# Optimization experiments

Measured on AMD Instinct MI355X. Metric: run time of the kernel, lower is better.

The kernel has to match this reference:

```python
import jax, jax.numpy as jnp
import numpy as np

N_NODES = 50000
N_EDGES = 1600000
E_DIM = 128
N_LAYERS = 3
N_GRAPHS = 32


def setup_inputs() -> dict:
    key = jax.random.key(0)
    ks = jax.random.split(key, 12)
    x = jax.random.normal(ks[0], (N_NODES,), dtype=jnp.float32)
    edge_index = jax.random.randint(ks[1], (2, N_EDGES), 0, N_NODES, dtype=jnp.int32)
    batch = jnp.sort(jax.random.randint(ks[2], (N_NODES,), 0, N_GRAPHS, dtype=jnp.int32))
    s_in = 1.0  # fan_in = 1 for the first linear
    s_e = 1.0 / np.sqrt(E_DIM)
    lin_w = jax.random.normal(ks[3], (1, E_DIM), jnp.float32) * s_in
    lin_b = jax.random.normal(ks[4], (E_DIM,), jnp.float32) * 0.01
    gcn_w = jax.random.normal(ks[5], (N_LAYERS, E_DIM, E_DIM), jnp.float32) * s_e
    gcn_b = jax.random.normal(ks[6], (N_LAYERS, E_DIM), jnp.float32) * 0.01
    r1_w = jax.random.normal(ks[7], (E_DIM, E_DIM), jnp.float32) * s_e
    r1_b = jax.random.normal(ks[8], (E_DIM,), jnp.float32) * 0.01
    r2_w = jax.random.normal(ks[9], (E_DIM, 1), jnp.float32) * s_e
    r2_b = jax.random.normal(ks[10], (1,), jnp.float32) * 0.01
    return {"x": x, "edge_index": edge_index, "batch": batch,
            "lin_w": lin_w, "lin_b": lin_b, "gcn_w": gcn_w, "gcn_b": gcn_b,
            "r1_w": r1_w, "r1_b": r1_b, "r2_w": r2_w, "r2_b": r2_b}


def reference(x, edge_index, batch, lin_w, lin_b, gcn_w, gcn_b, r1_w, r1_b, r2_w, r2_b):
    # input embedding: x.view(-1, 1) @ W + b -> [N, E]
    h = x.reshape(-1, 1) @ lin_w + lin_b

    # GCN normalization (add self-loops, symmetric deg^-1/2 norm) — structure is
    # identical across layers, so compute once.
    loops = jnp.arange(N_NODES, dtype=edge_index.dtype)
    src = jnp.concatenate([edge_index[0], loops])
    dst = jnp.concatenate([edge_index[1], loops])
    deg = jax.ops.segment_sum(jnp.ones(src.shape[0], h.dtype), dst, num_segments=N_NODES)
    dinv = jnp.where(deg > 0, jax.lax.rsqrt(deg), 0.0)
    norm = (dinv[src] * dinv[dst])[:, None]  # [E+N, 1]

    # NOTE: original calls x.relu() without assignment -> no activation (faithful).
    for l in range(N_LAYERS):
        h = h @ gcn_w[l]                                        # [N, E]
        h = jax.ops.segment_sum(h[src] * norm, dst, num_segments=N_NODES) + gcn_b[l]

    # global_add_pool over graphs
    pooled = jax.ops.segment_sum(h, batch, num_segments=N_GRAPHS)  # [G, E]
    hr = jnp.tanh(pooled @ r1_w + r1_b)
    return hr @ r2_w + r2_b  # [G, 1]
```

## Files before the change

kernel.cpp:

```cpp
#include <hip/hip_runtime.h>
#include <math.h>

#define NGRAPH 32
#define CAP 10240
#define EPT 8
#define EPB (256 * EPT)
#define BLK 256

__device__ __forceinline__ int block_scan_excl(int v, int tid, int* wsum, int& total) {
    int x = v;
#pragma unroll
    for (int d = 1; d < 64; d <<= 1) {
        int t = __shfl_up(x, d);
        if ((tid & 63) >= d) x += t;
    }
    if ((tid & 63) == 63) wsum[tid >> 6] = x;
    __syncthreads();
    if (tid == 0) {
        int a = 0;
#pragma unroll
        for (int i = 0; i < 4; i++) { int t = wsum[i]; wsum[i] = a; a += t; }
        wsum[4] = a;
    }
    __syncthreads();
    total = wsum[4];
    return x - v + wsum[tid >> 6];
}

__global__ __launch_bounds__(256) void k_part_chain(
        const int* __restrict__ src, const int* __restrict__ dst,
        int* __restrict__ gcursor, unsigned int* __restrict__ packed, int E, int nchunk,
        const float* __restrict__ lin_w, const float* __restrict__ lin_b,
        const float* __restrict__ gcn_w, const float* __restrict__ gcn_b,
        float* __restrict__ chainv) {
    __shared__ union {
        struct { unsigned int ldsbuf[EPB]; int hist[256], lofs[256], lcur[256], base[256], wsum[5]; } p;
        struct { float v4[512]; } c;
    } sm;
    int tid = threadIdx.x;

    if ((int)blockIdx.x == nchunk) {
        float* v4 = sm.c.v4;
        int j = tid & 127, gg = tid >> 7;
        if (tid < 128) {
            v4[tid]       = lin_w[tid];
            v4[128 + tid] = lin_b[tid];
            v4[256 + tid] = gcn_b[tid];
            v4[384 + tid] = gcn_b[128 + tid];
        }
        __syncthreads();
        for (int l = 0; l < 3; l++) {
            const float* W = gcn_w + l * 128 * 128;
            float a0 = 0.f, a1 = 0.f;
            for (int k0 = 0; k0 < 128; k0 += 16) {
                float wreg[16];
#pragma unroll
                for (int t = 0; t < 16; t++) wreg[t] = W[(k0 + t) * 128 + j];
#pragma unroll
                for (int t = 0; t < 16; t++) {
                    a0 += v4[gg * 128 + k0 + t] * wreg[t];
                    a1 += v4[(gg + 2) * 128 + k0 + t] * wreg[t];
                }
            }
            __syncthreads();
            v4[gg * 128 + j] = a0;
            bool upd = (gg == 0) ? (l >= 1) : (l >= 2);
            if (upd) v4[(gg + 2) * 128 + j] = a1;
            __syncthreads();
        }
        chainv[tid]       = v4[tid];
        chainv[256 + tid] = v4[256 + tid];
        return;
    }

    int e0 = blockIdx.x * EPB;
    sm.p.hist[tid] = 0;
    __syncthreads();
    int d_[EPT], s_[EPT];
#pragma unroll
    for (int c = 0; c < EPT / 4; c++) {
        int e = e0 + c * 1024 + (tid << 2);
        if (e + 3 < E) {
            int4 dv = *(const int4*)&dst[e];
            int4 sv = *(const int4*)&src[e];
            d_[4*c+0] = dv.x; d_[4*c+1] = dv.y; d_[4*c+2] = dv.z; d_[4*c+3] = dv.w;
            s_[4*c+0] = sv.x; s_[4*c+1] = sv.y; s_[4*c+2] = sv.z; s_[4*c+3] = sv.w;
            atomicAdd(&sm.p.hist[dv.x >> 8], 1);
            atomicAdd(&sm.p.hist[dv.y >> 8], 1);
            atomicAdd(&sm.p.hist[dv.z >> 8], 1);
            atomicAdd(&sm.p.hist[dv.w >> 8], 1);
        } else {
#pragma unroll
            for (int k = 0; k < 4; k++) {
                int ee = e + k;
                if (ee < E) {
                    d_[4*c+k] = dst[ee]; s_[4*c+k] = src[ee];
                    atomicAdd(&sm.p.hist[d_[4*c+k] >> 8], 1);
                } else {
                    d_[4*c+k] = -1;
                }
            }
        }
    }
    __syncthreads();
    int v = sm.p.hist[tid];
    int total;
    int excl = block_scan_excl(v, tid, sm.p.wsum, total);
    sm.p.lofs[tid] = excl;
    sm.p.lcur[tid] = excl;
    if (v > 0) sm.p.base[tid] = tid * CAP + atomicAdd(&gcursor[tid], v);
    __syncthreads();
#pragma unroll
    for (int c = 0; c < EPT; c++) {
        int dd = d_[c];
        if (dd >= 0) {
            int bk = dd >> 8;
            int slot = atomicAdd(&sm.p.lcur[bk], 1);
            sm.p.ldsbuf[slot] = ((unsigned int)bk << 24) | ((unsigned int)s_[c] << 8)
                              | (unsigned int)(dd & 255);
        }
    }
    __syncthreads();
    for (int i = tid; i < total; i += BLK) {
        unsigned int w = sm.p.ldsbuf[i];
        int bk = w >> 24;
        packed[sm.p.base[bk] + (i - sm.p.lofs[bk])] = w & 0xFFFFFFu;
    }
}

__global__ __launch_bounds__(256) void k_bucket(
        const unsigned int* __restrict__ packed, const int* __restrict__ gcursor,
        const float* __restrict__ x, const int* __restrict__ batch,
        int* __restrict__ offs, int* __restrict__ deg,
        float* __restrict__ dinv, float2* __restrict__ q0,
        float2* __restrict__ q1, float2* __restrict__ q2,
        unsigned short* __restrict__ csr, float* __restrict__ S, int N) {
    __shared__ unsigned int buf[CAP];
    __shared__ __align__(16) unsigned short lcsr[CAP];
    __shared__ int cnt[256], lcur[256], wsum[5];
    __shared__ float cs[NGRAPH];
    int tid = threadIdx.x;
    int b = blockIdx.x;
    int start = b * CAP;
    int len = gcursor[b];
    cnt[tid] = 0;
    if (tid < NGRAPH) cs[tid] = 0.f;
    __syncthreads();
    for (int e = tid; e < len; e += BLK) {
        unsigned int w = packed[start + e];
        buf[e] = w;
        atomicAdd(&cnt[w & 255], 1);
    }
    __syncthreads();
    int v = cnt[tid];
    int vp = (v + 7) & ~7;
    int total;
    int excl = block_scan_excl(vp, tid, wsum, total);
    lcur[tid] = excl;
    int node = b * 256 + tid;
    if (node < N) {
        deg[node] = v;
        offs[node] = start + excl;
        float dv = rsqrtf((float)(v + 1));
        dinv[node] = dv;
        q0[node] = make_float2(x[node] * dv, dv);
        atomicAdd(&cs[batch[node]], 1.f);
        for (int p = v; p < vp; p++)
            lcsr[excl + p] = (unsigned short)N;
    }
    if (b == 0 && tid == 0) {
        q0[N] = make_float2(0.f, 0.f);
        q1[N] = make_float2(0.f, 0.f);
        q2[N] = make_float2(0.f, 0.f);
    }
    __syncthreads();
    for (int e = tid; e < len; e += BLK) {
        unsigned int w = buf[e];
        lcsr[atomicAdd(&lcur[w & 255], 1)] = (unsigned short)(w >> 8);
    }
    if (tid < NGRAPH && cs[tid] != 0.f) atomicAdd(&S[tid], cs[tid]);
    __syncthreads();
    const uint4* ls = (const uint4*)lcsr;
    uint4* gs = (uint4*)&csr[start];
    for (int i = tid; i < (total >> 3); i += BLK) gs[i] = ls[i];
}

template <int WRITE_Q>
__global__ __launch_bounds__(256) void k_hop(
        const float2* __restrict__ qin, float2* __restrict__ outv,
        const unsigned short* __restrict__ csr,
        const int* __restrict__ offs, const int* __restrict__ deg,
        const float* __restrict__ dinv, int N) {
    int tid  = threadIdx.x;
    int lane = tid & 3;
    int node = blockIdx.x * 64 + (tid >> 2);
    if (node >= N) return;
    int e = offs[node], ne = deg[node];
    float sx = 0.0f, su = 0.0f;
    for (int j = 8 * lane; j < ne; j += 32) {
        ushort4 c0 = *(const ushort4*)&csr[e + j];
        ushort4 c1 = *(const ushort4*)&csr[e + j + 4];
        float2 a0 = qin[c0.x], a1 = qin[c0.y], a2 = qin[c0.z], a3 = qin[c0.w];
        float2 b0 = qin[c1.x], b1 = qin[c1.y], b2 = qin[c1.z], b3 = qin[c1.w];
        sx += ((a0.x + a1.x) + (a2.x + a3.x)) + ((b0.x + b1.x) + (b2.x + b3.x));
        su += ((a0.y + a1.y) + (a2.y + a3.y)) + ((b0.y + b1.y) + (b2.y + b3.y));
    }
#pragma unroll
    for (int m = 2; m > 0; m >>= 1) {
        sx += __shfl_xor(sx, m);
        su += __shfl_xor(su, m);
    }
    if (lane == 0) {
        float2 qs = qin[node];
        float dv = dinv[node];
        float px = dv * (sx + qs.x), pu = dv * (su + qs.y);
        if (WRITE_Q) outv[node] = make_float2(px * dv, pu * dv);
        else         outv[node] = make_float2(px, pu);
    }
}

__global__ __launch_bounds__(256) void k_mlp(
        const float* __restrict__ S, const float* __restrict__ chainv,
        const float2* __restrict__ q1, const float2* __restrict__ q2,
        const float2* __restrict__ p3, const float* __restrict__ dinv,
        const float* __restrict__ gcn_b,
        const float* __restrict__ r1_w, const float* __restrict__ r1_b,
        const float* __restrict__ r2_w, const float* __restrict__ r2_b,
        float* __restrict__ out, int N) {
    __shared__ float rw[128 * 128];
    __shared__ float pl[128], red[128];
    __shared__ float cnts[NGRAPH];
    __shared__ float r4[4 * 128];
    int tid = threadIdx.x;
    int g = blockIdx.x;
    {
        const float4* Rg = (const float4*)r1_w;
        float4* Rs = (float4*)rw;
#pragma unroll
        for (int i = 0; i < 16; i++) Rs[tid + i * 256] = Rg[tid + i * 256];
    }
    if (tid < NGRAPH) cnts[tid] = S[tid];
    __syncthreads();
    int r0 = 0;
    for (int i = 0; i < g; i++) r0 += (int)cnts[i];
    int cnt = (int)cnts[g];
    int r1e = r0 + cnt;
    float su1 = 0.f, su2 = 0.f, su3 = 0.f, sv3 = 0.f;
    for (int n = r0 + tid; n < r1e; n += BLK) {
        float inv = 1.0f / dinv[n];
        su1 += q1[n].y * inv;
        su2 += q2[n].y * inv;
        float2 p = p3[n];
        su3 += p.y; sv3 += p.x;
    }
#pragma unroll
    for (int m = 32; m > 0; m >>= 1) {
        su1 += __shfl_xor(su1, m);
        su2 += __shfl_xor(su2, m);
        su3 += __shfl_xor(su3, m);
        sv3 += __shfl_xor(sv3, m);
    }
    int wv = tid >> 6;
    if ((tid & 63) == 0) {
        r4[wv] = su1; r4[4 + wv] = su2; r4[8 + wv] = su3; r4[12 + wv] = sv3;
    }
    __syncthreads();
    su1 = r4[0] + r4[1] + r4[2] + r4[3];
    su2 = r4[4] + r4[5] + r4[6] + r4[7];
    su3 = r4[8] + r4[9] + r4[10] + r4[11];
    sv3 = r4[12] + r4[13] + r4[14] + r4[15];
    const float* b3 = gcn_b + 2 * 128;
    if (tid < 128)
        pl[tid] = sv3 * chainv[tid] + su3 * chainv[128 + tid] + su2 * chainv[256 + tid]
                + su1 * chainv[384 + tid] + (float)cnt * b3[tid];
    __syncthreads();
    int j = tid & 127, half = tid >> 7;
    float acc = 0.f;
#pragma unroll 8
    for (int kk = 0; kk < 64; kk++) {
        int k = half * 64 + kk;
        acc += pl[k] * rw[k * 128 + j];
    }
    r4[half * 128 + j] = acc;
    __syncthreads();
    if (tid < 128) {
        float a = r4[tid] + r4[128 + tid] + r1_b[tid];
        red[tid] = tanhf(a) * r2_w[tid];
    }
    __syncthreads();
    for (int sft = 64; sft > 0; sft >>= 1) {
        if (tid < sft) red[tid] += red[tid + sft];
        __syncthreads();
    }
    if (tid == 0) out[g] = red[0] + r2_b[0];
}

extern "C" void kernel_launch(void* const* d_in, const int* in_sizes, int n_in,
                              void* d_out, int out_size, void* d_ws, size_t ws_size,
                              hipStream_t stream) {
    const float* x     = (const float*)d_in[0];
    const int*   eidx  = (const int*)d_in[1];
    const int*   batch = (const int*)d_in[2];
    const float* lin_w = (const float*)d_in[3];
    const float* lin_b = (const float*)d_in[4];
    const float* gcn_w = (const float*)d_in[5];
    const float* gcn_b = (const float*)d_in[6];
    const float* r1_w  = (const float*)d_in[7];
    const float* r1_b  = (const float*)d_in[8];
    const float* r2_w  = (const float*)d_in[9];
    const float* r2_b  = (const float*)d_in[10];

    const int N = in_sizes[0];
    const int E = in_sizes[1] / 2;
    const int* src = eidx;
    const int* dst = eidx + E;
    const int NB = (N + 255) / 256;

    char* w = (char*)d_ws;
    float2* q0      = (float2*)w; w += (size_t)(N + 2) * 8;
    float2* q1      = (float2*)w; w += (size_t)(N + 2) * 8;
    float2* q2      = (float2*)w; w += (size_t)(N + 2) * 8;
    float2* p3      = (float2*)w; w += (size_t)(N + 2) * 8;
    unsigned int* packed = (unsigned int*)w; w += (size_t)256 * CAP * 4;
    int*    offs    = (int*)w;    w += (size_t)N * 4;
    int*    deg     = (int*)w;    w += (size_t)N * 4;
    float*  dinv    = (float*)w;  w += (size_t)N * 4;
    int*    gcursor = (int*)w;    w += 256 * 4;
    float*  S       = (float*)w;  w += 64 * 4;
    float*  chainv  = (float*)w;  w += 512 * 4;
    unsigned short* csr = (unsigned short*)w; w += (size_t)256 * CAP * 2 + 256;

    hipMemsetAsync(gcursor, 0, 256 * 4 + 64 * 4, stream);

    const int nchunk = (E + EPB - 1) / EPB;
    k_part_chain<<<nchunk + 1, 256, 0, stream>>>(src, dst, gcursor, packed, E, nchunk,
                                                 lin_w, lin_b, gcn_w, gcn_b, chainv);
    k_bucket<<<NB, 256, 0, stream>>>(packed, gcursor, x, batch, offs, deg, dinv,
                                     q0, q1, q2, csr, S, N);

    const int hop_blocks = (N + 63) / 64;
    k_hop<1><<<hop_blocks, 256, 0, stream>>>(q0, q1, csr, offs, deg, dinv, N);
    k_hop<1><<<hop_blocks, 256, 0, stream>>>(q1, q2, csr, offs, deg, dinv, N);
    k_hop<0><<<hop_blocks, 256, 0, stream>>>(q2, p3, csr, offs, deg, dinv, N);

    k_mlp<<<NGRAPH, 256, 0, stream>>>(S, chainv, q1, q2, p3, dinv, gcn_b,
                                      r1_w, r1_b, r2_w, r2_b, (float*)d_out, N);
}
```

Measured before the change: 155.7 us.

## Fuse per-graph pooling reductions into hop kernels via shared-memory atomics

The per-graph sums of q1, q2 and the final hop output are now accumulated inside the second and third hop kernels. Each block reduces into shared-memory bins keyed by the node's batch id, then adds the bins to a global array with atomics. This removes the p3 buffer write, the q1/q2/p3 re-reads and the serial per-graph scan in the MLP kernel. The MLP kernel also stops staging the 64KB r1_w matrix in LDS and reads it from global memory instead. The cost is atomic contention on 32 bins and a different floating-point summation order.

```diff
diff --git a/kernel.cpp b/kernel.cpp
--- a/kernel.cpp
+++ b/kernel.cpp
@@ -6,6 +6,7 @@
 #define EPT 8
 #define EPB (256 * EPT)
 #define BLK 256
+
 
 __device__ __forceinline__ int block_scan_excl(int v, int tid, int* wsum, int& total) {
     int x = v;
@@ -185,8 +186,7 @@
     for (int i = tid; i < (total >> 3); i += BLK) gs[i] = ls[i];
 }
 
-template <int WRITE_Q>
-__global__ __launch_bounds__(256) void k_hop(
+__global__ __launch_bounds__(256) void k_hop1(
         const float2* __restrict__ qin, float2* __restrict__ outv,
         const unsigned short* __restrict__ csr,
         const int* __restrict__ offs, const int* __restrict__ deg,
@@ -214,72 +214,122 @@
         float2 qs = qin[node];
         float dv = dinv[node];
         float px = dv * (sx + qs.x), pu = dv * (su + qs.y);
-        if (WRITE_Q) outv[node] = make_float2(px * dv, pu * dv);
-        else         outv[node] = make_float2(px, pu);
+        outv[node] = make_float2(px * dv, pu * dv);
+    }
+}
+
+__global__ __launch_bounds__(256) void k_hop2(
+        const float2* __restrict__ qin, float2* __restrict__ outv,
+        const unsigned short* __restrict__ csr,
+        const int* __restrict__ offs, const int* __restrict__ deg,
+        const float* __restrict__ dinv, const int* __restrict__ batch,
+        float* __restrict__ gsum, int N) {
+    __shared__ float aS[NGRAPH];
+    int tid  = threadIdx.x;
+    int lane = tid & 3;
+    int node = blockIdx.x * 64 + (tid >> 2);
+    if (tid < NGRAPH) aS[tid] = 0.f;
+    __syncthreads();
+    if (node < N) {
+        int e = offs[node], ne = deg[node];
+        float sx = 0.0f, su = 0.0f;
+        for (int j = 8 * lane; j < ne; j += 32) {
+            ushort4 c0 = *(const ushort4*)&csr[e + j];
+            ushort4 c1 = *(const ushort4*)&csr[e + j + 4];
+            float2 a0 = qin[c0.x], a1 = qin[c0.y], a2 = qin[c0.z], a3 = qin[c0.w];
+            float2 b0 = qin[c1.x], b1 = qin[c1.y], b2 = qin[c1.z], b3 = qin[c1.w];
+            sx += ((a0.x + a1.x) + (a2.x + a3.x)) + ((b0.x + b1.x) + (b2.x + b3.x));
+            su += ((a0.y + a1.y) + (a2.y + a3.y)) + ((b0.y + b1.y) + (b2.y + b3.y));
+        }
+#pragma unroll
+        for (int m = 2; m > 0; m >>= 1) {
+            sx += __shfl_xor(sx, m);
+            su += __shfl_xor(su, m);
+        }
+        if (lane == 0) {
+            float2 qs = qin[node];
+            float dv = dinv[node];
+            float px = dv * (sx + qs.x), pu = dv * (su + qs.y);
+            outv[node] = make_float2(px * dv, pu * dv);
+            atomicAdd(&aS[batch[node]], qs.y * (1.0f / dv));
+        }
+    }
+    __syncthreads();
+    if (tid < NGRAPH) {
+        float v = aS[tid];
+        if (v != 0.f) atomicAdd(&gsum[tid], v);
+    }
+}
+
+__global__ __launch_bounds__(256) void k_hop3(
+        const float2* __restrict__ qin,
+        const unsigned short* __restrict__ csr,
+        const int* __restrict__ offs, const int* __restrict__ deg,
+        const float* __restrict__ dinv, const int* __restrict__ batch,
+        float* __restrict__ gsum, int N) {
+    __shared__ float aS[NGRAPH], aV[NGRAPH], aU[NGRAPH];
+    int tid  = threadIdx.x;
+    int lane = tid & 3;
+    int node = blockIdx.x * 64 + (tid >> 2);
+    if (tid < NGRAPH) { aS[tid] = 0.f; aV[tid] = 0.f; aU[tid] = 0.f; }
+    __syncthreads();
+    if (node < N) {
+        int e = offs[node], ne = deg[node];
+        float sx = 0.0f, su = 0.0f;
+        for (int j = 8 * lane; j < ne; j += 32) {
+            ushort4 c0 = *(const ushort4*)&csr[e + j];
+            ushort4 c1 = *(const ushort4*)&csr[e + j + 4];
+            float2 a0 = qin[c0.x], a1 = qin[c0.y], a2 = qin[c0.z], a3 = qin[c0.w];
+            float2 b0 = qin[c1.x], b1 = qin[c1.y], b2 = qin[c1.z], b3 = qin[c1.w];
+            sx += ((a0.x + a1.x) + (a2.x + a3.x)) + ((b0.x + b1.x) + (b2.x + b3.x));
+            su += ((a0.y + a1.y) + (a2.y + a3.y)) + ((b0.y + b1.y) + (b2.y + b3.y));
+        }
+#pragma unroll
+        for (int m = 2; m > 0; m >>= 1) {
+            sx += __shfl_xor(sx, m);
+            su += __shfl_xor(su, m);
+        }
+        if (lane == 0) {
+            float2 qs = qin[node];
+            float dv = dinv[node];
+            float px = dv * (sx + qs.x), pu = dv * (su + qs.y);
+            int g = batch[node];
+            atomicAdd(&aS[g], qs.y * (1.0f / dv));
+            atomicAdd(&aV[g], px);
+            atomicAdd(&aU[g], pu);
+        }
+    }
+    __syncthreads();
+    if (tid < NGRAPH) {
+        float v;
+        v = aS[tid]; if (v != 0.f) atomicAdd(&gsum[32 + tid], v);
+        v = aV[tid]; if (v != 0.f) atomicAdd(&gsum[64 + tid], v);
+        v = aU[tid]; if (v != 0.f) atomicAdd(&gsum[96 + tid], v);
     }
 }
 
 __global__ __launch_bounds__(256) void k_mlp(
         const float* __restrict__ S, const float* __restrict__ chainv,
-        const float2* __restrict__ q1, const float2* __restrict__ q2,
-        const float2* __restrict__ p3, const float* __restrict__ dinv,
-        const float* __restrict__ gcn_b,
+        const float* __restrict__ gsum, const float* __restrict__ gcn_b,
         const float* __restrict__ r1_w, const float* __restrict__ r1_b,
         const float* __restrict__ r2_w, const float* __restrict__ r2_b,
-        float* __restrict__ out, int N) {
-    __shared__ float rw[128 * 128];
-    __shared__ float pl[128], red[128];
-    __shared__ float cnts[NGRAPH];
-    __shared__ float r4[4 * 128];
+        float* __restrict__ out) {
+    __shared__ float pl[128], red[128], r4[256];
     int tid = threadIdx.x;
     int g = blockIdx.x;
-    {
-        const float4* Rg = (const float4*)r1_w;
-        float4* Rs = (float4*)rw;
-#pragma unroll
-        for (int i = 0; i < 16; i++) Rs[tid + i * 256] = Rg[tid + i * 256];
-    }
-    if (tid < NGRAPH) cnts[tid] = S[tid];
-    __syncthreads();
-    int r0 = 0;
-    for (int i = 0; i < g; i++) r0 += (int)cnts[i];
-    int cnt = (int)cnts[g];
-    int r1e = r0 + cnt;
-    float su1 = 0.f, su2 = 0.f, su3 = 0.f, sv3 = 0.f;
-    for (int n = r0 + tid; n < r1e; n += BLK) {
-        float inv = 1.0f / dinv[n];
-        su1 += q1[n].y * inv;
-        su2 += q2[n].y * inv;
-        float2 p = p3[n];
-        su3 += p.y; sv3 += p.x;
-    }
-#pragma unroll
-    for (int m = 32; m > 0; m >>= 1) {
-        su1 += __shfl_xor(su1, m);
-        su2 += __shfl_xor(su2, m);
-        su3 += __shfl_xor(su3, m);
-        sv3 += __shfl_xor(sv3, m);
-    }
-    int wv = tid >> 6;
-    if ((tid & 63) == 0) {
-        r4[wv] = su1; r4[4 + wv] = su2; r4[8 + wv] = su3; r4[12 + wv] = sv3;
-    }
-    __syncthreads();
-    su1 = r4[0] + r4[1] + r4[2] + r4[3];
-    su2 = r4[4] + r4[5] + r4[6] + r4[7];
-    su3 = r4[8] + r4[9] + r4[10] + r4[11];
-    sv3 = r4[12] + r4[13] + r4[14] + r4[15];
+    float su1 = gsum[g], su2 = gsum[32 + g], sv3 = gsum[64 + g], su3 = gsum[96 + g];
+    float cnt = S[g];
     const float* b3 = gcn_b + 2 * 128;
     if (tid < 128)
         pl[tid] = sv3 * chainv[tid] + su3 * chainv[128 + tid] + su2 * chainv[256 + tid]
-                + su1 * chainv[384 + tid] + (float)cnt * b3[tid];
+                + su1 * chainv[384 + tid] + cnt * b3[tid];
     __syncthreads();
     int j = tid & 127, half = tid >> 7;
     float acc = 0.f;
 #pragma unroll 8
     for (int kk = 0; kk < 64; kk++) {
         int k = half * 64 + kk;
-        acc += pl[k] * rw[k * 128 + j];
+        acc += pl[k] * r1_w[k * 128 + j];
     }
     r4[half * 128 + j] = acc;
     __syncthreads();
@@ -320,17 +370,17 @@
     float2* q0      = (float2*)w; w += (size_t)(N + 2) * 8;
     float2* q1      = (float2*)w; w += (size_t)(N + 2) * 8;
     float2* q2      = (float2*)w; w += (size_t)(N + 2) * 8;
-    float2* p3      = (float2*)w; w += (size_t)(N + 2) * 8;
     unsigned int* packed = (unsigned int*)w; w += (size_t)256 * CAP * 4;
     int*    offs    = (int*)w;    w += (size_t)N * 4;
     int*    deg     = (int*)w;    w += (size_t)N * 4;
     float*  dinv    = (float*)w;  w += (size_t)N * 4;
     int*    gcursor = (int*)w;    w += 256 * 4;
     float*  S       = (float*)w;  w += 64 * 4;
+    float*  gsum    = (float*)w;  w += 128 * 4;
     float*  chainv  = (float*)w;  w += 512 * 4;
     unsigned short* csr = (unsigned short*)w; w += (size_t)256 * CAP * 2 + 256;
 
-    hipMemsetAsync(gcursor, 0, 256 * 4 + 64 * 4, stream);
+    hipMemsetAsync(gcursor, 0, 256 * 4 + 64 * 4 + 128 * 4, stream);
 
     const int nchunk = (E + EPB - 1) / EPB;
     k_part_chain<<<nchunk + 1, 256, 0, stream>>>(src, dst, gcursor, packed, E, nchunk,
@@ -339,10 +389,10 @@
                                      q0, q1, q2, csr, S, N);
 
     const int hop_blocks = (N + 63) / 64;
-    k_hop<1><<<hop_blocks, 256, 0, stream>>>(q0, q1, csr, offs, deg, dinv, N);
-    k_hop<1><<<hop_blocks, 256, 0, stream>>>(q1, q2, csr, offs, deg, dinv, N);
-    k_hop<0><<<hop_blocks, 256, 0, stream>>>(q2, p3, csr, offs, deg, dinv, N);
-
-    k_mlp<<<NGRAPH, 256, 0, stream>>>(S, chainv, q1, q2, p3, dinv, gcn_b,
-                                      r1_w, r1_b, r2_w, r2_b, (float*)d_out, N);
-}
+    k_hop1<<<hop_blocks, 256, 0, stream>>>(q0, q1, csr, offs, deg, dinv, N);
+    k_hop2<<<hop_blocks, 256, 0, stream>>>(q1, q2, csr, offs, deg, dinv, batch, gsum, N);
+    k_hop3<<<hop_blocks, 256, 0, stream>>>(q2, csr, offs, deg, dinv, batch, gsum, N);
+
+    k_mlp<<<NGRAPH, 256, 0, stream>>>(S, chainv, gsum, gcn_b,
+                                      r1_w, r1_b, r2_w, r2_b, (float*)d_out);
+}
```

Result: slower. 173.2 us (+11.2%).
